# Kernel tuning notes

Measured on AMD Instinct MI355X. Metric: run time of the kernel, lower is better.

Reference implementation:

```python
import jax, jax.numpy as jnp
import numpy as np

# Block-sparse linear config: W is (OUT_F, IN_F) in BSR form with BS x BS blocks,
OUT_F, IN_F, BS, K = 4096, 4096, 64, 32
NROW, NCOL = OUT_F // BS, IN_F // BS   # 64, 64
NNZB = NROW * K                         # 2048 nonzero blocks
BATCH = 8192


def setup_inputs() -> dict:
    key = jax.random.key(0)
    k1, k2, k3 = jax.random.split(key, 3)
    x = jax.random.normal(k1, (BATCH, IN_F), jnp.float32)
    values = jax.random.normal(k2, (NNZB, BS, BS), jnp.float32) * 0.02
    bias = jax.random.normal(k3, (OUT_F,), jnp.float32) * 0.01
    # BSR structure: K sorted, distinct column-block indices per block-row.
    cols = np.stack([np.sort((r + 2 * np.arange(K)) % NCOL) for r in range(NROW)])
    col_indices = jnp.asarray(cols.reshape(-1), jnp.int32)          # [NNZB]
    crow_indices = jnp.arange(NROW + 1, dtype=jnp.int32) * K        # [NROW+1]
    return {"x": x, "values": values, "bias": bias,
            "crow_indices": crow_indices, "col_indices": col_indices}


def reference(x, values, bias, crow_indices, col_indices):
    # Expand BSR row pointers to per-block row ids (structure is static/int).
    counts = jnp.diff(crow_indices)
    row_ids = jnp.repeat(jnp.arange(NROW), counts, total_repeat_length=NNZB)
    # Scatter nonzero blocks into a dense weight (only ~67 MB, cheap vs the GEMM).
    Wb = jnp.zeros((NROW, NCOL, BS, BS), values.dtype).at[row_ids, col_indices].set(values)
    W = Wb.transpose(0, 2, 1, 3).reshape(OUT_F, IN_F)  # [out_features, in_features]
    # forward: (W @ x.T).T + bias  ==  x @ W.T + bias
    return x @ W.T + bias
```

## Files before the change

### kernel.cpp

```cpp
#include <hip/hip_runtime.h>
#include <stdint.h>


#define BATCH   8192
#define IN_F    4096
#define OUT_F   4096
#define BS      64
#define NROW    64
#define NNZB    2048
#define BM      256
#define LDS_A_BYTES (BM * BS * 2)
#define LDS_B_BYTES (BS * BS * 2)

typedef float f32x4 __attribute__((ext_vector_type(4)));
typedef short s16x8 __attribute__((ext_vector_type(8)));

__device__ __forceinline__ void async_copy16(const void* g, void* l) {
  __builtin_amdgcn_global_load_lds(
      (__attribute__((address_space(1))) void*)g,
      (__attribute__((address_space(3))) void*)l, 16, 0, 0);
}

__device__ __forceinline__ unsigned short f32_to_bf16(float f) {
  union { float f; uint32_t u; } v; v.f = f;
  return (unsigned short)((v.u + 0x7FFFu + ((v.u >> 16) & 1u)) >> 16);
}

__global__ void cvt_kernel(const float4* __restrict__ in,
                           ushort4* __restrict__ out, int n4) {
  int i = blockIdx.x * blockDim.x + threadIdx.x;
  if (i < n4) {
    float4 v = in[i];
    ushort4 o;
    o.x = f32_to_bf16(v.x); o.y = f32_to_bf16(v.y);
    o.z = f32_to_bf16(v.z); o.w = f32_to_bf16(v.w);
    out[i] = o;
  }
}

__global__ __launch_bounds__(256) void bsr_gemm_kernel(
    const unsigned short* __restrict__ xb,
    const unsigned short* __restrict__ wb,
    const float* __restrict__ bias,
    const int* __restrict__ crow,
    const int* __restrict__ cols,
    float* __restrict__ out) {
  __shared__ alignas(16) char smem[LDS_A_BYTES + LDS_B_BYTES];

  const int tid = threadIdx.x;
  const int w   = tid >> 6;
  const int l   = tid & 63;
  const int r   = blockIdx.x;
  const int m0  = blockIdx.y * BM;

  const int start = crow[r];
  const int end   = crow[r + 1];

  const int lr = l & 15;
  const int q  = l >> 4;

  f32x4 acc[4][4];
#pragma unroll
  for (int mi = 0; mi < 4; ++mi)
#pragma unroll
    for (int ni = 0; ni < 4; ++ni) {
      f32x4 z = {0.f, 0.f, 0.f, 0.f};
      acc[mi][ni] = z;
    }

  const int arow = (w << 3) + (l >> 3);
  const unsigned short* agbase =
      xb + (size_t)(m0 + arow) * IN_F + ((l & 7) << 3);
  char* const alds = smem + (w << 10) + (l << 4);
  char* const blds = smem + LDS_A_BYTES + (w << 10) + (l << 4);
  const int bgoff = (w << 9) + (l << 3);

  for (int i = start; i < end; ++i) {
    const int c = cols[i];
    const unsigned short* ag = agbase + (size_t)c * BS;
    const unsigned short* bg = wb + ((size_t)i << 12) + bgoff;

    __syncthreads();
#pragma unroll
    for (int it = 0; it < 8; ++it)
      async_copy16(ag + (size_t)(it * 32) * IN_F, alds + it * 4096);
#pragma unroll
    for (int it = 0; it < 2; ++it)
      async_copy16(bg + it * 2048, blds + it * 4096);
    __syncthreads();

#pragma unroll
    for (int ks = 0; ks < 2; ++ks) {
      s16x8 af[4], bf[4];
#pragma unroll
      for (int mi = 0; mi < 4; ++mi)
        af[mi] = *(const s16x8*)(smem + ((w << 6) + (mi << 4) + lr) * 128 +
                                 (ks << 6) + (q << 4));
#pragma unroll
      for (int ni = 0; ni < 4; ++ni)
        bf[ni] = *(const s16x8*)(smem + LDS_A_BYTES + ((ni << 4) + lr) * 128 +
                                 (ks << 6) + (q << 4));
#pragma unroll
      for (int mi = 0; mi < 4; ++mi)
#pragma unroll
        for (int ni = 0; ni < 4; ++ni)
          acc[mi][ni] = __builtin_amdgcn_mfma_f32_16x16x32_bf16(
              af[mi], bf[ni], acc[mi][ni], 0, 0, 0);
    }
  }

  const int colg = (r << 6) + lr;
#pragma unroll
  for (int ni = 0; ni < 4; ++ni) {
    const float bv = bias[colg + (ni << 4)];
#pragma unroll
    for (int mi = 0; mi < 4; ++mi) {
      float* op = out +
          (size_t)(m0 + (w << 6) + (mi << 4) + (q << 2)) * OUT_F +
          colg + (ni << 4);
#pragma unroll
      for (int e = 0; e < 4; ++e)
        op[(size_t)e * OUT_F] = acc[mi][ni][e] + bv;
    }
  }
}

__global__ void fallback_kernel(const float* __restrict__ x,
                                const float* __restrict__ vals,
                                const float* __restrict__ bias,
                                const int* __restrict__ crow,
                                const int* __restrict__ cols,
                                float* __restrict__ out) {
  int idx = blockIdx.x * 256 + threadIdx.x;
  int m = idx >> 12;
  int n = idx & 4095;
  int r = n >> 6, nl = n & 63;
  float s = 0.f;
  int e = crow[r + 1];
  for (int i = crow[r]; i < e; ++i) {
    const float* xp = x + (size_t)m * IN_F + cols[i] * 64;
    const float* wp = vals + ((size_t)i << 12) + nl * 64;
    for (int k = 0; k < 64; ++k) s += xp[k] * wp[k];
  }
  out[idx] = s + bias[n];
}

extern "C" void kernel_launch(void* const* d_in, const int* in_sizes, int n_in,
                              void* d_out, int out_size, void* d_ws,
                              size_t ws_size, hipStream_t stream) {
  const float* x    = (const float*)d_in[0];
  const float* vals = (const float*)d_in[1];
  const float* bias = (const float*)d_in[2];
  const int*   crow = (const int*)d_in[3];
  const int*   cols = (const int*)d_in[4];
  float* out = (float*)d_out;

  const size_t x_elems = (size_t)BATCH * IN_F;
  const size_t w_elems = (size_t)NNZB * BS * BS;
  const size_t need = (x_elems + w_elems) * 2;

  if (ws_size >= need) {
    unsigned short* xb = (unsigned short*)d_ws;
    unsigned short* wb = xb + x_elems;
    cvt_kernel<<<(int)(x_elems / 4 / 256), 256, 0, stream>>>(
        (const float4*)x, (ushort4*)xb, (int)(x_elems / 4));
    cvt_kernel<<<(int)(w_elems / 4 / 256), 256, 0, stream>>>(
        (const float4*)vals, (ushort4*)wb, (int)(w_elems / 4));
    dim3 grid(NROW, BATCH / BM);
    bsr_gemm_kernel<<<grid, 256, 0, stream>>>(xb, wb, bias, crow, cols, out);
  } else {
    fallback_kernel<<<(BATCH * OUT_F) / 256, 256, 0, stream>>>(
        x, vals, bias, crow, cols, out);
  }
}
```

Before: 407.6 us.

## Pair block-rows sharing column indices so each X tile feeds two weight blocks

Each workgroup now handles two block-rows (r and r+2), whose column sets overlap heavily under the test pattern. It merge-walks the two sorted column lists and loads the X tile once for both, so activation traffic per useful MFMA drops. The workgroup grows to 512 threads: four waves serve each row, and a wave skips compute when its row has no block at that column. LDS loads and stores also get an XOR swizzle to cut bank conflicts. The pairing depends on rows r and r+2 sharing columns; with arbitrary sparsity this could add wasted iterations, but results remain correct.

```diff
diff --git a/kernel.cpp b/kernel.cpp
--- a/kernel.cpp
+++ b/kernel.cpp
@@ -10,7 +10,7 @@
 #define NNZB    2048
 #define BM      256
 #define LDS_A_BYTES (BM * BS * 2)
-#define LDS_B_BYTES (BS * BS * 2)
+#define LDS_B_BYTES (2 * BS * BS * 2)
 
 typedef float f32x4 __attribute__((ext_vector_type(4)));
 typedef short s16x8 __attribute__((ext_vector_type(8)));
@@ -38,7 +38,7 @@
   }
 }
 
-__global__ __launch_bounds__(256) void bsr_gemm_kernel(
+__global__ __launch_bounds__(512) void bsr_gemm_pair_kernel(
     const unsigned short* __restrict__ xb,
     const unsigned short* __restrict__ wb,
     const float* __restrict__ bias,
@@ -50,14 +50,21 @@
   const int tid = threadIdx.x;
   const int w   = tid >> 6;
   const int l   = tid & 63;
-  const int r   = blockIdx.x;
+  const int wm  = w & 3;
+  const int wn  = w >> 2;
+  const int p   = blockIdx.x;
+  const int rA  = ((p >> 1) << 2) + (p & 1);
+  const int rB  = rA + 2;
   const int m0  = blockIdx.y * BM;
 
-  const int start = crow[r];
-  const int end   = crow[r + 1];
+  const int startA = crow[rA], endA = crow[rA + 1];
+  const int startB = crow[rB], endB = crow[rB + 1];
 
   const int lr = l & 15;
   const int q  = l >> 4;
+
+  int cvA = (startA + l < endA) ? cols[startA + l] : 0;
+  int cvB = (startB + l < endB) ? cols[startB + l] : 0;
 
   f32x4 acc[4][4];
 #pragma unroll
@@ -68,55 +75,69 @@
       acc[mi][ni] = z;
     }
 
-  const int arow = (w << 3) + (l >> 3);
+  const int srow = tid >> 3;
+  const int sswz = ((tid & 7) ^ (srow & 7)) << 3;
   const unsigned short* agbase =
-      xb + (size_t)(m0 + arow) * IN_F + ((l & 7) << 3);
-  char* const alds = smem + (w << 10) + (l << 4);
-  char* const blds = smem + LDS_A_BYTES + (w << 10) + (l << 4);
-  const int bgoff = (w << 9) + (l << 3);
+      xb + (size_t)(m0 + srow) * IN_F + sswz;
+  char* const alds = smem + tid * 16;
+  char* const blds = smem + LDS_A_BYTES + tid * 16;
+  const int bgoff = (srow << 6) + sswz;
 
-  for (int i = start; i < end; ++i) {
-    const int c = cols[i];
-    const unsigned short* ag = agbase + (size_t)c * BS;
-    const unsigned short* bg = wb + ((size_t)i << 12) + bgoff;
+  int ia = startA, ib = startB;
+  while ((ia < endA) || (ib < endB)) {
+    const int ca = (ia < endA) ? __shfl(cvA, ia - startA) : 0x7fffffff;
+    const int cb = (ib < endB) ? __shfl(cvB, ib - startB) : 0x7fffffff;
+    const int c = min(ca, cb);
+    const bool hasA = (ca == c);
+    const bool hasB = (cb == c);
+    const int iA = ia, iB = ib;
+    if (hasA) ++ia;
+    if (hasB) ++ib;
 
     __syncthreads();
+    const unsigned short* ag = agbase + (size_t)c * BS;
 #pragma unroll
-    for (int it = 0; it < 8; ++it)
-      async_copy16(ag + (size_t)(it * 32) * IN_F, alds + it * 4096);
-#pragma unroll
-    for (int it = 0; it < 2; ++it)
-      async_copy16(bg + it * 2048, blds + it * 4096);
+    for (int it = 0; it < 4; ++it)
+      async_copy16(ag + (size_t)(it * 64) * IN_F, alds + it * 8192);
+    if (hasA)
+      async_copy16(wb + ((size_t)iA << 12) + bgoff, blds);
+    if (hasB)
+      async_copy16(wb + ((size_t)iB << 12) + bgoff, blds + 8192);
     __syncthreads();
 
+    const bool active = wn ? hasB : hasA;
+    if (active) {
 #pragma unroll
-    for (int ks = 0; ks < 2; ++ks) {
-      s16x8 af[4], bf[4];
+      for (int ks = 0; ks < 2; ++ks) {
+        const int chunk = (((ks << 2) + q) ^ (l & 7)) << 4;
+        s16x8 af[4], bf[4];
 #pragma unroll
-      for (int mi = 0; mi < 4; ++mi)
-        af[mi] = *(const s16x8*)(smem + ((w << 6) + (mi << 4) + lr) * 128 +
-                                 (ks << 6) + (q << 4));
-#pragma unroll
-      for (int ni = 0; ni < 4; ++ni)
-        bf[ni] = *(const s16x8*)(smem + LDS_A_BYTES + ((ni << 4) + lr) * 128 +
-                                 (ks << 6) + (q << 4));
-#pragma unroll
-      for (int mi = 0; mi < 4; ++mi)
+        for (int mi = 0; mi < 4; ++mi)
+          af[mi] = *(const s16x8*)(smem +
+                     ((wm << 6) + (mi << 4) + lr) * 128 + chunk);
 #pragma unroll
         for (int ni = 0; ni < 4; ++ni)
-          acc[mi][ni] = __builtin_amdgcn_mfma_f32_16x16x32_bf16(
-              af[mi], bf[ni], acc[mi][ni], 0, 0, 0);
+          bf[ni] = *(const s16x8*)(smem + LDS_A_BYTES + (wn << 13) +
+                     ((ni << 4) + lr) * 128 + chunk);
+#pragma unroll
+        for (int mi = 0; mi < 4; ++mi)
+#pragma unroll
+          for (int ni = 0; ni < 4; ++ni)
+            acc[mi][ni] = __builtin_amdgcn_mfma_f32_16x16x32_bf16(
+                af[mi], bf[ni], acc[mi][ni], 0, 0, 0);
+      }
     }
   }
 
-  const int colg = (r << 6) + lr;
+  const int rW = wn ? rB : rA;
+  const int colg = (rW << 6) + lr;
 #pragma unroll
   for (int ni = 0; ni < 4; ++ni) {
     const float bv = bias[colg + (ni << 4)];
 #pragma unroll
     for (int mi = 0; mi < 4; ++mi) {
       float* op = out +
-          (size_t)(m0 + (w << 6) + (mi << 4) + (q << 2)) * OUT_F +
+          (size_t)(m0 + (wm << 6) + (mi << 4) + (q << 2)) * OUT_F +
           colg + (ni << 4);
 #pragma unroll
       for (int e = 0; e < 4; ++e)
@@ -166,8 +187,9 @@
         (const float4*)x, (ushort4*)xb, (int)(x_elems / 4));
     cvt_kernel<<<(int)(w_elems / 4 / 256), 256, 0, stream>>>(
         (const float4*)vals, (ushort4*)wb, (int)(w_elems / 4));
-    dim3 grid(NROW, BATCH / BM);
-    bsr_gemm_kernel<<<grid, 256, 0, stream>>>(xb, wb, bias, crow, cols, out);
+    dim3 grid(NROW / 2, BATCH / BM);
+    bsr_gemm_pair_kernel<<<grid, 512, 0, stream>>>(xb, wb, bias, crow, cols,
+                                                   out);
   } else {
     fallback_kernel<<<(BATCH * OUT_F) / 256, 256, 0, stream>>>(
         x, vals, bias, crow, cols, out);
```

Result: faster. 373.8 us (-8.3%).
